# Kernel tuning notes

Measured on AMD Instinct MI355X. Metric: run time of the kernel, lower is better.

## Reference

```python
import jax, jax.numpy as jnp
import numpy as np

N, G, CIN, COUT, K, M, H, W = 4, 8, 256, 256, 3, 4, 32, 32


def setup_inputs() -> dict:
    key = jax.random.key(0)
    ks = jax.random.split(key, 12)
    s = 0.02
    return {
        "x": jax.random.normal(ks[0], (N, G, CIN, H, W), jnp.float32),
        # grouped 1x1 conv weights: (G, out_per_group, in_per_group)
        "wq": jax.random.normal(ks[1], (G, COUT, CIN), jnp.float32) * s,
        "wk": jax.random.normal(ks[2], (G, COUT, CIN), jnp.float32) * s,
        "wv": jax.random.normal(ks[3], (G, COUT, CIN), jnp.float32) * s,
        # relative embeddings: height varies over K1, width over K2
        "hm": jax.random.normal(ks[4], (G * COUT // 2, K, 1), jnp.float32),
        "wm": jax.random.normal(ks[5], (G * COUT // 2, 1, K), jnp.float32),
        "w_conv": jax.random.normal(ks[6], (G, CIN, COUT), jnp.float32) * s,
        "b_conv": jnp.zeros((G, CIN), jnp.float32),
        "w_f1": jax.random.normal(ks[7], (G, COUT, CIN), jnp.float32) * s,
        "b_f1": jnp.zeros((G, COUT), jnp.float32),
        "w_f2": jax.random.normal(ks[8], (G, CIN, COUT), jnp.float32) * s,
        "b_f2": jnp.zeros((G, CIN), jnp.float32),
        "g1": jnp.ones((CIN // M,), jnp.float32),
        "b1": jnp.zeros((CIN // M,), jnp.float32),
        "g2": jnp.ones((CIN // M,), jnp.float32),
        "b2": jnp.zeros((CIN // M,), jnp.float32),
    }


def _gconv(x, w, b=None):
    # grouped 1x1 conv: x (N,G,Ci,H,W), w (G,Co,Ci)
    y = jnp.einsum('ngihw,goi->ngohw', x, w)
    return y if b is None else y + b[None, :, :, None, None]


def _unfold(x4, k):
    # nn.Unfold(k, 1, (k-1)//2, 1): x4 (N,C,H,W) -> patches (N,C,k,k,H,W)
    p = (k - 1) // 2
    hh, ww = x4.shape[2], x4.shape[3]
    xp = jnp.pad(x4, ((0, 0), (0, 0), (p, p), (p, p)))
    return jnp.stack(
        [jnp.stack([xp[:, :, i:i + hh, j:j + ww] for j in range(k)], axis=2)
         for i in range(k)], axis=2)


def _skip(t, m):
    # 'N G (M D) H W -> N (H W) M G D'
    n, g, c, h, w = t.shape
    d = c // m
    return t.reshape(n, g, m, d, h, w).transpose(0, 4, 5, 2, 1, 3).reshape(n, h * w, m, g, d)


def _ln(t, gamma, beta, eps=1e-5):
    mu = t.mean(-1, keepdims=True)
    var = t.var(-1, keepdims=True)  # biased, matches torch LayerNorm
    return (t - mu) / jnp.sqrt(var + eps) * gamma + beta


def _forward(x, wq, wk, wv, hm, wm, w_conv, b_conv, w_f1, b_f1, w_f2, b_f2, g1, b1, g2, b2):
    n, g, c, h, w = x.shape
    m = M
    dout = COUT // m
    q = _gconv(x, wq).reshape(n, g, m, dout, h, w)
    k0 = _gconv(x, wk).reshape(n, g * COUT, h, w)
    kp = _unfold(k0, K)  # (n, G*COUT, K, K, h, w)
    half = g * COUT // 2
    kp = jnp.concatenate(
        [kp[:, :half] + hm[None, :, :, :, None, None],
         kp[:, half:] + wm[None, :, :, :, None, None]], axis=1)
    kp = kp.reshape(n, g, m, dout, K, K, h, w)
    v0 = _gconv(x, wv).reshape(n, g * COUT, h, w)
    vp = _unfold(v0, K).reshape(n, g, m, dout, K, K, h, w)
    # per (pixel, head): q (G,D) @ k (D, G*KK) -> softmax -> @ v (G*KK, D)
    scores = jnp.einsum('ngmdhw,nemdijhw->nhwmgeij', q, kp)
    attn = jax.nn.softmax(scores.reshape(n, h, w, m, g, -1), axis=-1)
    attn = attn.reshape(n, h, w, m, g, g, K, K)
    av = jnp.einsum('nhwmgeij,nemdijhw->ngmdhw', attn, vp)
    y = av.reshape(n, g, m * dout, h, w)
    y = _gconv(y, w_conv, b_conv)  # (n, g, CIN, h, w)
    t = _ln(_skip(x, m) + _skip(y, m), g1, b1)  # (n, hw, m, g, d)
    # NB: source does .reshape (not a permute) here -> intentional layout scramble
    y = t.reshape(n, g, -1, h, w)
    f = _gconv(jax.nn.relu(_gconv(y, w_f1, b_f1)), w_f2, b_f2)
    t2 = _ln(_skip(y, m) + _skip(f, m), g2, b2)
    return t2.reshape(n, g, -1, h, w)


def reference(x, wq, wk, wv, hm, wm, w_conv, b_conv, w_f1, b_f1, w_f2, b_f2, g1, b1, g2, b2):
    return _forward(x, wq, wk, wv, hm, wm, w_conv, b_conv, w_f1, b_f1, w_f2, b_f2, g1, b1, g2, b2)
```

## Files before the change

kernel.cpp:

```cpp
#include <hip/hip_runtime.h>


typedef unsigned short u16;
typedef unsigned int u32;
typedef __attribute__((ext_vector_type(8))) short bf16x8;
typedef __attribute__((ext_vector_type(4))) float f32x4;

__device__ __forceinline__ u32 fbits(float f) { u32 x; __builtin_memcpy(&x, &f, 4); return x; }
__device__ __forceinline__ float bf2f(u32 v) {
    u32 x = v << 16; float f; __builtin_memcpy(&f, &x, 4); return f;
}
__device__ __forceinline__ u16 f2bf(float f) {
    u32 x = fbits(f);
    u32 r = x + 0x7fffu + ((x >> 16) & 1u);
    return (u16)(r >> 16);
}
__device__ __forceinline__ u32 pack2bf(float a, float b) {
    return __builtin_amdgcn_perm(fbits(b) + 0x8000u, fbits(a) + 0x8000u, 0x07060302u);
}

__device__ __forceinline__ void unpack8(uint4 u, float* o) {
    o[0] = bf2f(u.x & 0xffff); o[1] = bf2f(u.x >> 16);
    o[2] = bf2f(u.y & 0xffff); o[3] = bf2f(u.y >> 16);
    o[4] = bf2f(u.z & 0xffff); o[5] = bf2f(u.z >> 16);
    o[6] = bf2f(u.w & 0xffff); o[7] = bf2f(u.w >> 16);
}
__device__ __forceinline__ void ld8bf(const u16* p, float* o) { unpack8(*(const uint4*)p, o); }
__device__ __forceinline__ void ld8f(const float* p, float* o) {
    float4 a = *(const float4*)p, b = *(const float4*)(p + 4);
    o[0] = a.x; o[1] = a.y; o[2] = a.z; o[3] = a.w;
    o[4] = b.x; o[5] = b.y; o[6] = b.z; o[7] = b.w;
}
__device__ __forceinline__ void st4bf(u16* p, const float* v) {
    ushort4 s; s.x = f2bf(v[0]); s.y = f2bf(v[1]); s.z = f2bf(v[2]); s.w = f2bf(v[3]);
    *(ushort4*)p = s;
}

#if defined(__has_builtin)
#if __has_builtin(__builtin_amdgcn_fdot2_f32_bf16)
#define HAVE_BFDOT 1
#endif
#endif
#ifdef HAVE_BFDOT
typedef __attribute__((ext_vector_type(2))) __bf16 v2bf;
__device__ __forceinline__ float dot2bf(u32 a, u32 b, float c) {
    return __builtin_amdgcn_fdot2_f32_bf16(__builtin_bit_cast(v2bf, a),
                                           __builtin_bit_cast(v2bf, b), c, false);
}
#else
__device__ __forceinline__ float dot2bf(u32 a, u32 b, float c) {
    return c + bf2f(a & 0xffff) * bf2f(b & 0xffff) + bf2f(a >> 16) * bf2f(b >> 16);
}
#endif
__device__ __forceinline__ float dot8bf(uint4 a, uint4 b, float c) {
    c = dot2bf(a.x, b.x, c); c = dot2bf(a.y, b.y, c);
    c = dot2bf(a.z, b.z, c); c = dot2bf(a.w, b.w, c);
    return c;
}

typedef const __attribute__((address_space(1))) u32 glob_u32;
typedef __attribute__((address_space(3))) u32 lds_u32;

__device__ __forceinline__ void gl16(const void* g, void* l) {
    __builtin_amdgcn_global_load_lds((glob_u32*)g, (lds_u32*)l, 16, 0, 0);
}

__global__ __launch_bounds__(256) void rel_kernel(const float* __restrict__ hm,
                                                  const float* __restrict__ wm,
                                                  u16* __restrict__ relT) {
    const int t = threadIdx.x;
    const int c0 = t << 3;
    const float* rb = (t < 128) ? (hm + (size_t)c0 * 3)
                                : (wm + (size_t)(c0 - 1024) * 3);
    float r[24];
    #pragma unroll
    for (int q = 0; q < 6; q++) {
        float4 f = *(const float4*)(rb + q * 4);
        r[q * 4] = f.x; r[q * 4 + 1] = f.y; r[q * 4 + 2] = f.z; r[q * 4 + 3] = f.w;
    }
    #pragma unroll
    for (int idx = 0; idx < 3; idx++) {
        u32 pk[4];
        #pragma unroll
        for (int j = 0; j < 4; j++)
            pk[j] = pack2bf(r[(2 * j) * 3 + idx], r[(2 * j + 1) * 3 + idx]);
        *(uint4*)(relT + idx * 2048 + c0) = *(uint4*)pk;
    }
}

template<int BMODE, int OM, int RELU, int RF32>
__global__ __launch_bounds__(256) void gemm_kernel(
    const float* __restrict__ A0, const float* __restrict__ A1,
    const float* __restrict__ A2, const void* __restrict__ B,
    const float* __restrict__ bias, const void* __restrict__ resid,
    const float* __restrict__ gamma, const float* __restrict__ beta,
    u16* __restrict__ O0, u16* __restrict__ O1, u16* __restrict__ O2) {
    __shared__ __align__(16) char smem[OM >= 2 ? 37376 : (OM == 1 ? 33792 : 20480)];
    u16* Al = (u16*)smem;
    u16* Bl = (u16*)(smem + 10240);
    float* Cl = (float*)smem;
    float* red  = (float*)(smem + 33792);
    float* mu_s = (float*)(smem + 35840);
    float* rs_s = (float*)(smem + 36352);
    float* g_s  = (float*)(smem + 36864);
    float* b_s  = (float*)(smem + 37120);

    const int tid = threadIdx.x;
    const int pt = blockIdx.x, ot = blockIdx.y;
    const int ngz = blockIdx.z, sel = ngz >> 5, ng = ngz & 31;
    const float* A = (sel == 0) ? A0 : (sel == 1) ? A1 : A2;
    u16* out      = (sel == 0) ? O0 : (sel == 1) ? O1 : O2;
    const int n = ng >> 3, g = ng & 7;
    const int p0 = pt << 7, o0 = ot << 7;
    const float* Ag = A + (size_t)g * 65536;

    if (OM >= 2 && tid < 64) { g_s[tid] = gamma[tid]; b_s[tid] = beta[tid]; }

    const int l = tid & 63, w = tid >> 6;
    const int mq = w >> 1;
    const int mw = mq << 6, nw = (w & 1) << 6;
    const int lrow = l & 15, lk = (l >> 4) << 3;

    f32x4 acc[4][4];
    #pragma unroll
    for (int i = 0; i < 4; i++)
        #pragma unroll
        for (int j = 0; j < 4; j++) acc[i][j] = (f32x4){0.f, 0.f, 0.f, 0.f};

    for (int k0 = 0; k0 < 256; k0 += 32) {
        {
            const int r = tid >> 1, cb = (tid & 1) << 4;
            const float* src = Ag + (size_t)(o0 + r) * 256 + k0 + cb;
            u32* dst = (u32*)&Al[r * 40 + cb];
            #pragma unroll
            for (int q = 0; q < 4; q++) {
                float4 f = *(const float4*)(src + q * 4);
                dst[q * 2]     = pack2bf(f.x, f.y);
                dst[q * 2 + 1] = pack2bf(f.z, f.w);
            }
        }
        if (BMODE == 2) {
            const int r = tid >> 1, cb = (tid & 1) << 4;
            const int k = k0 + cb;
            const int cmaj = ((k >> 6) << 9) + g * 64 + (k & 63);
            const u16* src = (const u16*)B + (size_t)(n * 1024 + p0 + r) * 2048 + cmaj;
            *(uint4*)&Bl[r * 40 + cb]     = *(const uint4*)src;
            *(uint4*)&Bl[r * 40 + cb + 8] = *(const uint4*)(src + 8);
        } else if (BMODE == 1) {
            const int kp = tid & 15, po = tid >> 4;
            const u16* src = (const u16*)B + (size_t)(ng * 256 + k0 + 2 * kp) * 1024 + p0 + po * 8;
            uint4 r0 = *(const uint4*)src;
            uint4 r1 = *(const uint4*)(src + 1024);
            u32 a0[4] = { r0.x, r0.y, r0.z, r0.w };
            u32 a1[4] = { r1.x, r1.y, r1.z, r1.w };
            #pragma unroll
            for (int j = 0; j < 4; j++) {
                u32 w0 = __builtin_amdgcn_perm(a1[j], a0[j], 0x05040100u);
                u32 w1 = __builtin_amdgcn_perm(a1[j], a0[j], 0x07060302u);
                *(u32*)&Bl[(po * 8 + 2 * j    ) * 40 + 2 * kp] = w0;
                *(u32*)&Bl[(po * 8 + 2 * j + 1) * 40 + 2 * kp] = w1;
            }
        } else {
            const int kp = tid & 15, po = tid >> 4;
            const float* src = (const float*)B + (size_t)(ng * 256 + k0 + 2 * kp) * 1024 + p0 + po * 8;
            float r0[8], r1[8];
            ld8f(src, r0); ld8f(src + 1024, r1);
            #pragma unroll
            for (int j = 0; j < 8; j++)
                *(u32*)&Bl[(po * 8 + j) * 40 + 2 * kp] = pack2bf(r0[j], r1[j]);
        }
        __syncthreads();
        bf16x8 af[4], bfg[4];
        #pragma unroll
        for (int i = 0; i < 4; i++) af[i]  = *(const bf16x8*)&Al[(mw + i * 16 + lrow) * 40 + lk];
        #pragma unroll
        for (int j = 0; j < 4; j++) bfg[j] = *(const bf16x8*)&Bl[(nw + j * 16 + lrow) * 40 + lk];
        #pragma unroll
        for (int i = 0; i < 4; i++)
            #pragma unroll
            for (int j = 0; j < 4; j++)
                acc[i][j] = __builtin_amdgcn_mfma_f32_16x16x32_bf16(af[i], bfg[j], acc[i][j], 0, 0, 0);
        __syncthreads();
    }

    if (OM == 0) {
        #pragma unroll
        for (int i = 0; i < 4; i++) {
            const int orow = o0 + mw + i * 16 + ((l >> 4) << 2);
            const int cmaj = ((orow >> 6) << 9) + g * 64 + (orow & 63);
            #pragma unroll
            for (int j = 0; j < 4; j++) {
                const int p = p0 + nw + j * 16 + lrow;
                float v4[4] = { acc[i][j].x, acc[i][j].y, acc[i][j].z, acc[i][j].w };
                st4bf(out + (size_t)(n * 1024 + p) * 2048 + cmaj, v4);
            }
        }
    } else if (OM == 1) {
        for (int ph = 0; ph < 2; ph++) {
            __syncthreads();
            if (mq == ph) {
                #pragma unroll
                for (int i = 0; i < 4; i++) {
                    const int rl = i * 16 + ((l >> 4) << 2);
                    #pragma unroll
                    for (int j = 0; j < 4; j++) {
                        const int c = nw + j * 16 + lrow;
                        Cl[(rl    ) * 132 + c] = acc[i][j].x;
                        Cl[(rl + 1) * 132 + c] = acc[i][j].y;
                        Cl[(rl + 2) * 132 + c] = acc[i][j].z;
                        Cl[(rl + 3) * 132 + c] = acc[i][j].w;
                    }
                }
            }
            __syncthreads();
            {
                const int row = tid >> 2, pc = (tid & 3) << 5;
                const int og = o0 + ph * 64 + row;
                const float bb = bias ? bias[g * 256 + og] : 0.f;
                u32 pk[16];
                #pragma unroll
                for (int q = 0; q < 8; q++) {
                    float4 f = *(const float4*)&Cl[row * 132 + pc + q * 4];
                    float a0 = f.x + bb, a1 = f.y + bb, a2 = f.z + bb, a3 = f.w + bb;
                    if (RELU) {
                        a0 = fmaxf(a0, 0.f); a1 = fmaxf(a1, 0.f);
                        a2 = fmaxf(a2, 0.f); a3 = fmaxf(a3, 0.f);
                    }
                    pk[q * 2]     = pack2bf(a0, a1);
                    pk[q * 2 + 1] = pack2bf(a2, a3);
                }
                u16* dst = out + (size_t)(ng * 256 + og) * 1024 + p0 + pc;
                #pragma unroll
                for (int q = 0; q < 4; q++) *(uint4*)(dst + q * 8) = *(uint4*)&pk[q * 4];
            }
        }
    } else {
        for (int ph = 0; ph < 2; ph++) {
            const int ms = (ot << 1) | ph;
            __syncthreads();
            if (mq == ph) {
                #pragma unroll
                for (int i = 0; i < 4; i++) {
                    const int rl = i * 16 + ((l >> 4) << 2);
                    #pragma unroll
                    for (int j = 0; j < 4; j++) {
                        const int c = nw + j * 16 + lrow;
                        Cl[(rl    ) * 132 + c] = acc[i][j].x;
                        Cl[(rl + 1) * 132 + c] = acc[i][j].y;
                        Cl[(rl + 2) * 132 + c] = acc[i][j].z;
                        Cl[(rl + 3) * 132 + c] = acc[i][j].w;
                    }
                }
            }
            __syncthreads();
            {
                const int row = tid >> 2, pc = (tid & 3) << 5;
                const int o = (ms << 6) + row;
                const float bb = bias[g * 256 + o];
                const size_t rb = (size_t)(ng * 256 + o) * 1024 + p0 + pc;
                float* cp = &Cl[row * 132 + pc];
                #pragma unroll
                for (int c8 = 0; c8 < 4; c8++) {
                    float r8[8];
                    if (RF32) ld8f((const float*)resid + rb + c8 * 8, r8);
                    else      ld8bf((const u16*)resid + rb + c8 * 8, r8);
                    #pragma unroll
                    for (int u = 0; u < 8; u++) cp[c8 * 8 + u] += bb + r8[u];
                }
            }
            __syncthreads();
            {
                const int c = tid & 127, hh = tid >> 7;
                float sm = 0.f, sq = 0.f;
                #pragma unroll
                for (int r = 0; r < 32; r++) {
                    float v = Cl[(hh * 32 + r) * 132 + c];
                    sm += v; sq += v * v;
                }
                red[hh * 128 + c] = sm; red[256 + hh * 128 + c] = sq;
            }
            __syncthreads();
            if (tid < 128) {
                float s2 = red[tid] + red[128 + tid];
                float q2 = red[256 + tid] + red[384 + tid];
                float mu = s2 * (1.f / 64.f);
                float var = q2 * (1.f / 64.f) - mu * mu;
                mu_s[tid] = mu; rs_s[tid] = rsqrtf(var + 1e-5f);
            }
            __syncthreads();
            {
                const int c = tid & 127, dh = (tid >> 7) << 5;
                const float mu = mu_s[c], rs = rs_s[c];
                const size_t ob = (size_t)n * 2097152 + (size_t)(p0 + c) * 2048
                                + ms * 512 + g * 64 + dh;
                if (OM == 3) {
                    float* op = (float*)O0 + ob;
                    #pragma unroll
                    for (int q4 = 0; q4 < 8; q4++) {
                        float4 f;
                        f.x = (Cl[(dh + q4 * 4    ) * 132 + c] - mu) * rs * g_s[dh + q4 * 4    ] + b_s[dh + q4 * 4    ];
                        f.y = (Cl[(dh + q4 * 4 + 1) * 132 + c] - mu) * rs * g_s[dh + q4 * 4 + 1] + b_s[dh + q4 * 4 + 1];
                        f.z = (Cl[(dh + q4 * 4 + 2) * 132 + c] - mu) * rs * g_s[dh + q4 * 4 + 2] + b_s[dh + q4 * 4 + 2];
                        f.w = (Cl[(dh + q4 * 4 + 3) * 132 + c] - mu) * rs * g_s[dh + q4 * 4 + 3] + b_s[dh + q4 * 4 + 3];
                        *(float4*)(op + q4 * 4) = f;
                    }
                } else {
                    u16* op = O0 + ob;
                    #pragma unroll
                    for (int q8 = 0; q8 < 4; q8++) {
                        u32 pk[4];
                        #pragma unroll
                        for (int j = 0; j < 4; j++) {
                            const int d = dh + q8 * 8 + j * 2;
                            float a = (Cl[(d    ) * 132 + c] - mu) * rs * g_s[d    ] + b_s[d    ];
                            float b = (Cl[(d + 1) * 132 + c] - mu) * rs * g_s[d + 1] + b_s[d + 1];
                            pk[j] = pack2bf(a, b);
                        }
                        *(uint4*)(op + q8 * 8) = *(uint4*)pk;
                    }
                }
            }
        }
    }
}

__global__ __launch_bounds__(256, 4) void attn_kernel(
    const u16* __restrict__ qt, const u16* __restrict__ kt,
    const u16* __restrict__ vt, const u16* __restrict__ relT,
    u16* __restrict__ av) {
    __shared__ __align__(16) char kvb[9 * 4096];
    const int tid = threadIdx.x;
    const int bx = blockIdx.x, n = blockIdx.y;
    const int p = ((bx & 7) << 7) | (bx >> 3);
    const int ph = p >> 5, pw = p & 31;
    const size_t nimg = (size_t)n * 1024;

    int npix[9]; unsigned inb = 0;
    #pragma unroll
    for (int ij = 0; ij < 9; ij++) {
        int hs = ph + ij / 3 - 1, wc = pw + ij % 3 - 1;
        npix[ij] = hs * 32 + wc;
        if (((unsigned)hs < 32u) && ((unsigned)wc < 32u)) inb |= (1u << ij);
    }

    const int e_th = tid & 7, g_th = (tid >> 3) & 7, m_th = tid >> 6;
    const int l = tid & 63;
    const int e_l = l >> 3, d8_l = l & 7;
    const int gsw = m_th * 512 + e_l * 64 + ((d8_l ^ e_l) & 7) * 8;
    char* ldst = kvb + m_th * 1024;

    #pragma unroll
    for (int ij = 0; ij < 9; ij++)
        if (inb & (1u << ij))
            gl16(kt + (nimg + npix[ij]) * 2048 + gsw, ldst + ij * 4096);

    uint4 qv[8];
    {
        const u16* qp = qt + (nimg + p) * 2048 + m_th * 512 + g_th * 64;
        #pragma unroll
        for (int c8 = 0; c8 < 8; c8++) qv[c8] = *(const uint4*)(qp + c8 * 8);
    }

    float qrel3[3] = {};
    {
        const int ckr = e_th * 256 + m_th * 64;
        #pragma unroll
        for (int idx = 0; idx < 3; idx++)
            #pragma unroll
            for (int c8 = 0; c8 < 8; c8++) {
                uint4 rv = *(const uint4*)(relT + idx * 2048 + ckr + c8 * 8);
                qrel3[idx] = dot8bf(qv[c8], rv, qrel3[idx]);
            }
    }

    asm volatile("s_waitcnt vmcnt(0)" ::: "memory");

    float sc[9] = {};
    const int qkb = m_th * 1024 + e_th * 128;
    #pragma unroll
    for (int c8 = 0; c8 < 8; c8++) {
        const int sw = ((c8 ^ e_th) & 7) << 4;
        #pragma unroll
        for (int ij = 0; ij < 9; ij++)
            if (inb & (1u << ij)) {
                uint4 kv = *(const uint4*)(kvb + ij * 4096 + qkb + sw);
                sc[ij] = dot8bf(qv[c8], kv, sc[ij]);
            }
    }

    asm volatile("s_waitcnt lgkmcnt(0)" ::: "memory");
    #pragma unroll
    for (int ij = 0; ij < 9; ij++)
        if (inb & (1u << ij))
            gl16(vt + (nimg + npix[ij]) * 2048 + gsw, ldst + ij * 4096);

    #pragma unroll
    for (int ij = 0; ij < 9; ij++)
        sc[ij] += qrel3[(e_th < 4) ? (ij / 3) : (ij % 3)];

    float mx = sc[0];
    #pragma unroll
    for (int ij = 1; ij < 9; ij++) mx = fmaxf(mx, sc[ij]);
    mx = fmaxf(mx, __shfl_xor(mx, 1));
    mx = fmaxf(mx, __shfl_xor(mx, 2));
    mx = fmaxf(mx, __shfl_xor(mx, 4));
    float sum = 0.f;
    #pragma unroll
    for (int ij = 0; ij < 9; ij++) { sc[ij] = __expf(sc[ij] - mx); sum += sc[ij]; }
    sum += __shfl_xor(sum, 1); sum += __shfl_xor(sum, 2); sum += __shfl_xor(sum, 4);
    const float rinv = 1.f / sum;
    #pragma unroll
    for (int ij = 0; ij < 9; ij++) sc[ij] *= rinv;

    asm volatile("s_waitcnt vmcnt(0)" ::: "memory");

    const int db = l & 7, srcb = l & 0x38;
    const int avb = m_th * 1024;
    float acc[8] = {};
    #pragma unroll
    for (int ij = 0; ij < 9; ij++) {
        if (!(inb & (1u << ij))) continue;
        #pragma unroll
        for (int e = 0; e < 8; e++) {
            const float a = __shfl(sc[ij], srcb | e);
            uint4 vv = *(const uint4*)(kvb + ij * 4096 + avb + e * 128 + (((db ^ e) & 7) << 4));
            float v8[8];
            unpack8(vv, v8);
            #pragma unroll
            for (int u = 0; u < 8; u++) acc[u] += a * v8[u];
        }
    }
    const int c0 = m_th * 512 + (l >> 3) * 64 + (l & 7) * 8;
    st4bf(av + (nimg + p) * 2048 + c0, acc);
    st4bf(av + (nimg + p) * 2048 + c0 + 4, acc + 4);
}

extern "C" void kernel_launch(void* const* d_in, const int* in_sizes, int n_in,
                              void* d_out, int out_size, void* d_ws, size_t ws_size,
                              hipStream_t stream) {
    const float* x   = (const float*)d_in[0];
    const float* wq  = (const float*)d_in[1];
    const float* wk  = (const float*)d_in[2];
    const float* wv  = (const float*)d_in[3];
    const float* hm  = (const float*)d_in[4];
    const float* wm  = (const float*)d_in[5];
    const float* wc  = (const float*)d_in[6];
    const float* bc  = (const float*)d_in[7];
    const float* wf1 = (const float*)d_in[8];
    const float* bf1 = (const float*)d_in[9];
    const float* wf2 = (const float*)d_in[10];
    const float* bf2w = (const float*)d_in[11];
    const float* g1  = (const float*)d_in[12];
    const float* b1  = (const float*)d_in[13];
    const float* g2  = (const float*)d_in[14];
    const float* b2  = (const float*)d_in[15];
    char* ws = (char*)d_ws;
    u16* bufQ = (u16*)d_out;
    u16* relT = bufQ + 8388608;
    u16* bufK = (u16*)(ws);
    u16* bufV = (u16*)(ws + 16777216);

    const dim3 gg(8, 2, 32), gq(8, 2, 96), gb(256);
    rel_kernel<<<dim3(1), gb, 0, stream>>>(hm, wm, relT);
    gemm_kernel<3, 0, 0, 0><<<gq, gb, 0, stream>>>(
        wq, wk, wv, x, nullptr, nullptr, nullptr, nullptr, bufQ, bufK, bufV);
    attn_kernel<<<dim3(1024, 4), gb, 0, stream>>>(bufQ, bufK, bufV, relT, bufQ);
    gemm_kernel<2, 2, 0, 1><<<gg, gb, 0, stream>>>(
        wc, wc, wc, bufQ, bc, x, g1, b1, bufV, bufV, bufV);
    gemm_kernel<1, 1, 1, 0><<<gg, gb, 0, stream>>>(
        wf1, wf1, wf1, bufV, bf1, nullptr, nullptr, nullptr, bufK, bufK, bufK);
    gemm_kernel<1, 3, 0, 0><<<gg, gb, 0, stream>>>(
        wf2, wf2, wf2, bufK, bf2w, bufV, g2, b2,
        (u16*)d_out, (u16*)d_out, (u16*)d_out);
}
```

Before: 332.2 us.

## Pipeline K/V neighbor loads in stages, stage relative embeddings through LDS

Restructures the attention kernel into a staged software pipeline. The rel embeddings are loaded into LDS via async global-to-LDS copies, then K rows are loaded in two batches and V rows in two batches, each overlapping with dot-product compute on previously landed data, with explicit vmcnt waits and scheduling barriers. Out-of-bounds neighbors are clamped to valid pixels so loads are unconditional, and the rel layout is permuted to match the LDS swizzle. It also raises wave priority during the AV accumulation. The risks are extra redundant loads at image borders and tighter LDS reuse hazards between stages.

```diff
diff --git a/kernel.cpp b/kernel.cpp
--- a/kernel.cpp
+++ b/kernel.cpp
@@ -78,13 +78,14 @@
         float4 f = *(const float4*)(rb + q * 4);
         r[q * 4] = f.x; r[q * 4 + 1] = f.y; r[q * 4 + 2] = f.z; r[q * 4 + 3] = f.w;
     }
+    const int obase = ((c0 >> 6) & 3) * 512 + (c0 >> 8) * 64 + (c0 & 63);
     #pragma unroll
     for (int idx = 0; idx < 3; idx++) {
         u32 pk[4];
         #pragma unroll
         for (int j = 0; j < 4; j++)
             pk[j] = pack2bf(r[(2 * j) * 3 + idx], r[(2 * j + 1) * 3 + idx]);
-        *(uint4*)(relT + idx * 2048 + c0) = *(uint4*)pk;
+        *(uint4*)(relT + idx * 2048 + obase) = *(uint4*)pk;
     }
 }
 
@@ -324,6 +325,7 @@
     }
 }
 
+#define SBAR() __builtin_amdgcn_sched_barrier(0)
 __global__ __launch_bounds__(256, 4) void attn_kernel(
     const u16* __restrict__ qt, const u16* __restrict__ kt,
     const u16* __restrict__ vt, const u16* __restrict__ relT,
@@ -335,24 +337,23 @@
     const int ph = p >> 5, pw = p & 31;
     const size_t nimg = (size_t)n * 1024;
 
-    int npix[9]; unsigned inb = 0;
+    int cpix[9]; unsigned inb = 0;
     #pragma unroll
     for (int ij = 0; ij < 9; ij++) {
         int hs = ph + ij / 3 - 1, wc = pw + ij % 3 - 1;
-        npix[ij] = hs * 32 + wc;
         if (((unsigned)hs < 32u) && ((unsigned)wc < 32u)) inb |= (1u << ij);
+        int hc = hs < 0 ? 0 : (hs > 31 ? 31 : hs);
+        int wcl = wc < 0 ? 0 : (wc > 31 ? 31 : wc);
+        cpix[ij] = hc * 32 + wcl;
     }
 
     const int e_th = tid & 7, g_th = (tid >> 3) & 7, m_th = tid >> 6;
     const int l = tid & 63;
     const int e_l = l >> 3, d8_l = l & 7;
-    const int gsw = m_th * 512 + e_l * 64 + ((d8_l ^ e_l) & 7) * 8;
+    const int gsw = e_l * 64 + ((d8_l ^ e_l) & 7) * 8;
     char* ldst = kvb + m_th * 1024;
-
-    #pragma unroll
-    for (int ij = 0; ij < 9; ij++)
-        if (inb & (1u << ij))
-            gl16(kt + (nimg + npix[ij]) * 2048 + gsw, ldst + ij * 4096);
+    const u16* kb = kt + nimg * 2048 + m_th * 512 + gsw;
+    const u16* vb = vt + nimg * 2048 + m_th * 512 + gsw;
 
     uint4 qv[8];
     {
@@ -360,39 +361,71 @@
         #pragma unroll
         for (int c8 = 0; c8 < 8; c8++) qv[c8] = *(const uint4*)(qp + c8 * 8);
     }
-
+    SBAR();
+    #pragma unroll
+    for (int idx = 0; idx < 3; idx++)
+        gl16(relT + idx * 2048 + m_th * 512 + gsw, ldst + idx * 4096);
+    SBAR();
+    #pragma unroll
+    for (int ij = 3; ij < 9; ij++)
+        gl16(kb + (size_t)cpix[ij] * 2048, ldst + ij * 4096);
+    SBAR();
+    asm volatile("s_waitcnt vmcnt(6)" ::: "memory");
+    SBAR();
     float qrel3[3] = {};
-    {
-        const int ckr = e_th * 256 + m_th * 64;
-        #pragma unroll
-        for (int idx = 0; idx < 3; idx++)
-            #pragma unroll
-            for (int c8 = 0; c8 < 8; c8++) {
-                uint4 rv = *(const uint4*)(relT + idx * 2048 + ckr + c8 * 8);
-                qrel3[idx] = dot8bf(qv[c8], rv, qrel3[idx]);
-            }
-    }
-
-    asm volatile("s_waitcnt vmcnt(0)" ::: "memory");
-
-    float sc[9] = {};
     const int qkb = m_th * 1024 + e_th * 128;
     #pragma unroll
     for (int c8 = 0; c8 < 8; c8++) {
         const int sw = ((c8 ^ e_th) & 7) << 4;
         #pragma unroll
-        for (int ij = 0; ij < 9; ij++)
+        for (int idx = 0; idx < 3; idx++) {
+            uint4 rv = *(const uint4*)(kvb + idx * 4096 + qkb + sw);
+            qrel3[idx] = dot8bf(qv[c8], rv, qrel3[idx]);
+        }
+    }
+    asm volatile("s_waitcnt lgkmcnt(0)" ::: "memory");
+    SBAR();
+    #pragma unroll
+    for (int ij = 0; ij < 3; ij++)
+        gl16(kb + (size_t)cpix[ij] * 2048, ldst + ij * 4096);
+    SBAR();
+    asm volatile("s_waitcnt vmcnt(3)" ::: "memory");
+    SBAR();
+    float sc[9] = {};
+    #pragma unroll
+    for (int c8 = 0; c8 < 8; c8++) {
+        const int sw = ((c8 ^ e_th) & 7) << 4;
+        #pragma unroll
+        for (int ij = 3; ij < 9; ij++)
             if (inb & (1u << ij)) {
                 uint4 kv = *(const uint4*)(kvb + ij * 4096 + qkb + sw);
                 sc[ij] = dot8bf(qv[c8], kv, sc[ij]);
             }
     }
-
     asm volatile("s_waitcnt lgkmcnt(0)" ::: "memory");
-    #pragma unroll
-    for (int ij = 0; ij < 9; ij++)
-        if (inb & (1u << ij))
-            gl16(vt + (nimg + npix[ij]) * 2048 + gsw, ldst + ij * 4096);
+    SBAR();
+    #pragma unroll
+    for (int ij = 3; ij < 9; ij++)
+        gl16(vb + (size_t)cpix[ij] * 2048, ldst + ij * 4096);
+    SBAR();
+    asm volatile("s_waitcnt vmcnt(6)" ::: "memory");
+    SBAR();
+    #pragma unroll
+    for (int c8 = 0; c8 < 8; c8++) {
+        const int sw = ((c8 ^ e_th) & 7) << 4;
+        #pragma unroll
+        for (int ij = 0; ij < 3; ij++)
+            if (inb & (1u << ij)) {
+                uint4 kv = *(const uint4*)(kvb + ij * 4096 + qkb + sw);
+                sc[ij] = dot8bf(qv[c8], kv, sc[ij]);
+            }
+    }
+    asm volatile("s_waitcnt lgkmcnt(0)" ::: "memory");
+    SBAR();
+    #pragma unroll
+    for (int ij = 0; ij < 3; ij++)
+        gl16(vb + (size_t)cpix[ij] * 2048, ldst + ij * 4096);
+    SBAR();
 
     #pragma unroll
     for (int ij = 0; ij < 9; ij++)
@@ -413,7 +446,9 @@
     for (int ij = 0; ij < 9; ij++) sc[ij] *= rinv;
 
     asm volatile("s_waitcnt vmcnt(0)" ::: "memory");
-
+    SBAR();
+
+    __builtin_amdgcn_s_setprio(1);
     const int db = l & 7, srcb = l & 0x38;
     const int avb = m_th * 1024;
     float acc[8] = {};
@@ -430,10 +465,12 @@
             for (int u = 0; u < 8; u++) acc[u] += a * v8[u];
         }
     }
+    __builtin_amdgcn_s_setprio(0);
     const int c0 = m_th * 512 + (l >> 3) * 64 + (l & 7) * 8;
     st4bf(av + (nimg + p) * 2048 + c0, acc);
     st4bf(av + (nimg + p) * 2048 + c0 + 4, acc + 4);
 }
+#undef SBAR
 
 extern "C" void kernel_launch(void* const* d_in, const int* in_sizes, int n_in,
                               void* d_out, int out_size, void* d_ws, size_t ws_size,
```

Result: faster. 318.5 us (median of 2 runs) (-4.1%).
